# Kernel optimization log

Measured on AMD Instinct MI355X. Metric: run time of the kernel, lower is better.

Reference implementation:

```python
import jax, jax.numpy as jnp
import numpy as np

E = 128          # embed_dim / d_model
DI = 2 * E       # d_inner = expand * d_model = 256
H = 8            # nheads = d_inner / headdim
P = 32           # headdim
N = 64           # d_state
DC = 4           # d_conv
G = 1            # ngroups
XBC = DI + 2 * G * N            # 384
DIN = 2 * DI + 2 * G * N + H    # 648 in_proj width
NL = 4           # number of Mamba2 blocks
PS = 16          # patch size
EPS = 1e-5


def _silu(x):
    return x * jax.nn.sigmoid(x)


def _ln(x, w, b):
    mu = jnp.mean(x, axis=-1, keepdims=True)
    var = jnp.mean(jnp.square(x - mu), axis=-1, keepdims=True)
    return (x - mu) * jax.lax.rsqrt(var + EPS) * w + b


def setup_inputs() -> dict:
    key = jax.random.key(0)
    ks = jax.random.split(key, 20)
    B, IMG = 256, 256
    s = 0.02
    inp = {
        "x": jax.random.normal(ks[0], (B, 3, IMG, IMG), jnp.float32),
        # patch embed conv (E, 3, PS, PS) + bias, then LayerNorm
        "conv_w": jax.random.normal(ks[1], (E, 3, PS, PS), jnp.float32) * s,
        "conv_b": jnp.zeros((E,), jnp.float32),
        "pe_ln_w": jnp.ones((E,), jnp.float32),
        "pe_ln_b": jnp.zeros((E,), jnp.float32),
        # per-block LayerNorms (stacked over NL layers)
        "ln_w": jnp.ones((NL, E), jnp.float32),
        "ln_b": jnp.zeros((NL, E), jnp.float32),
        # Mamba2 params stacked over layers
        "in_w": jax.random.normal(ks[2], (NL, DIN, E), jnp.float32) * s,
        "conv1d_w": jax.random.normal(ks[3], (NL, XBC, DC), jnp.float32) * s,
        "conv1d_b": jnp.zeros((NL, XBC), jnp.float32),
        "dt_bias": jax.random.normal(ks[4], (NL, H), jnp.float32) * 0.5,
        "A_log": jnp.tile(jnp.log(jnp.arange(1, H + 1, dtype=jnp.float32)), (NL, 1)),
        "Dp": jnp.ones((NL, H), jnp.float32),
        "ssm_norm_w": jnp.ones((NL, DI), jnp.float32),
        "out_w": jax.random.normal(ks[5], (NL, E, DI), jnp.float32) * s,
        # final norm + head
        "fn_w": jnp.ones((E,), jnp.float32),
        "fn_b": jnp.zeros((E,), jnp.float32),
        "head_w": jax.random.normal(ks[6], (128, E), jnp.float32) * s,
        "head_b": jnp.zeros((128,), jnp.float32),
    }
    return inp


def _mamba2(x, in_w, cw, cb, dtb, A_log, Dp, nw, ow):
    B, L, _ = x.shape
    zxbcdt = jnp.einsum('ble,de->bld', x, in_w)          # [B,L,648]
    z = zxbcdt[..., :DI]                                  # [B,L,256]
    xbc = zxbcdt[..., DI:DI + XBC]                        # [B,L,384]
    dt = jax.nn.softplus(zxbcdt[..., DI + XBC:] + dtb)    # [B,L,H]
    # causal depthwise conv1d over seq, kernel DC, + silu
    xp = jnp.pad(xbc, ((0, 0), (DC - 1, 0), (0, 0)))
    conv = cb + sum(cw[:, k] * xp[:, k:k + L, :] for k in range(DC))
    xbc = _silu(conv)
    xh = xbc[..., :DI].reshape(B, L, H, P)                # [B,L,H,P]
    Bm = xbc[..., DI:DI + N]                              # [B,L,N] (g=1)
    Cm = xbc[..., DI + N:]                                # [B,L,N]
    A = -jnp.exp(A_log)                                   # [H]
    dA = jnp.exp(dt * A)                                  # [B,L,H]
    # sequential selective scan over L
    def step(h, t):
        dAt, dtt, xt, Bt, Ct = t
        h = dAt[..., None, None] * h + (dtt[..., None] * xt)[..., None] * Bt[:, None, None, :]
        y = jnp.einsum('bhpn,bn->bhp', h, Ct)
        return h, y
    h0 = jnp.zeros((B, H, P, N), x.dtype)
    xs = (jnp.moveaxis(dA, 1, 0), jnp.moveaxis(dt, 1, 0), jnp.moveaxis(xh, 1, 0),
          jnp.moveaxis(Bm, 1, 0), jnp.moveaxis(Cm, 1, 0))
    _, ys = jax.lax.scan(step, h0, xs)                    # [L,B,H,P]
    y = jnp.moveaxis(ys, 0, 1) + Dp[:, None] * xh         # [B,L,H,P]
    y = y.reshape(B, L, DI)
    # gated RMSNorm: rmsnorm(y * silu(z)) * weight
    y = y * _silu(z)
    y = y * jax.lax.rsqrt(jnp.mean(jnp.square(y), axis=-1, keepdims=True) + EPS) * nw
    return jnp.einsum('bld,ed->ble', y, ow)


def reference(x, conv_w, conv_b, pe_ln_w, pe_ln_b, ln_w, ln_b, in_w, conv1d_w,
              conv1d_b, dt_bias, A_log, Dp, ssm_norm_w, out_w, fn_w, fn_b,
              head_w, head_b):
    B = x.shape[0]
    Hh = x.shape[2] // PS
    Ww = x.shape[3] // PS
    # non-overlapping patch conv == blocked einsum
    xp = x.reshape(B, 3, Hh, PS, Ww, PS)
    t = jnp.einsum('bcxpyq,ecpq->bxye', xp, conv_w) + conv_b
    t = t.reshape(B, Hh * Ww, E)                          # [B,L,E]
    t = _ln(t, pe_ln_w, pe_ln_b)
    for i in range(NL):
        t = t + _mamba2(_ln(t, ln_w[i], ln_b[i]), in_w[i], conv1d_w[i],
                        conv1d_b[i], dt_bias[i], A_log[i], Dp[i],
                        ssm_norm_w[i], out_w[i])
    t = _ln(t, fn_w, fn_b)
    t = jnp.mean(t, axis=1)                               # [B,E]
    t = jnp.einsum('be,oe->bo', t, head_w) + head_b       # [B,128]
    nrm = jnp.maximum(jnp.linalg.norm(t, axis=1, keepdims=True), 1e-12)
    return t / nrm
```

## Files before the change

### kernel.cpp

```cpp
#include <hip/hip_runtime.h>
#include <math.h>

#define EE 128
#define DI 256
#define HH 8
#define PP 32
#define NN 64
#define DC 4
#define XBC 384
#define DIN 648
#define NL 4
#define LSEQ 256
#define BB 256
#define TTOK (BB * LSEQ)
#define EPSF 1e-5f

typedef __attribute__((ext_vector_type(8))) short short8;
typedef __attribute__((ext_vector_type(4))) float f32x4;

__device__ inline short f2bf(float f) {
  unsigned u = __builtin_bit_cast(unsigned, f);
  u += 0x7fff + ((u >> 16) & 1);
  return (short)(u >> 16);
}
__device__ inline float bf2f(unsigned short u) {
  unsigned x = ((unsigned)u) << 16;
  return __builtin_bit_cast(float, x);
}
__device__ inline float fast_silu(float a) {
  return a * __builtin_amdgcn_rcpf(1.f + __expf(-a));
}

__global__ __launch_bounds__(256) void cvt_w_kernel(
    const float* __restrict__ in_w, const float* __restrict__ ow,
    unsigned short* __restrict__ in_wb, unsigned short* __restrict__ owb) {
  int i = blockIdx.x * 256 + threadIdx.x;
  in_wb[i] = (unsigned short)f2bf(in_w[i]);
  if (i < NL * EE * DI) owb[i] = (unsigned short)f2bf(ow[i]);
}

__global__ __launch_bounds__(256) void gemm_in_proj(
    const unsigned short* __restrict__ A, const unsigned short* __restrict__ B,
    unsigned short* __restrict__ Czx, float* __restrict__ dtraw,
    int M, int N, int K) {
  __shared__ __align__(16) unsigned short smem[128 * 136];
  short (*As)[40] = (short(*)[40])smem;
  short (*Bs)[40] = (short(*)[40])(smem + 128 * 40);
  const int tid = threadIdx.x;
  const int lane = tid & 63, wid = tid >> 6;
  const int wm = wid >> 1, wn = wid & 1;
  const int m0 = blockIdx.y * 128, n0 = blockIdx.x * 128;
  const int r = tid >> 1, hf = tid & 1;
  const int lr = lane & 15, lk = (lane >> 4) * 8;
  f32x4 acc[4][4] = {};
  for (int k0 = 0; k0 < K; k0 += 32) {
    {
      const unsigned short* ap = A + (size_t)(m0 + r) * K + k0 + hf * 16;
      *(short8*)&As[r][hf * 16] = *(const short8*)(ap);
      *(short8*)&As[r][hf * 16 + 8] = *(const short8*)(ap + 8);
    }
    {
      short8 s0 = {}, s1 = {};
      if (n0 + r < N) {
        const unsigned short* bp = B + (size_t)(n0 + r) * K + k0 + hf * 16;
        s0 = *(const short8*)(bp);
        s1 = *(const short8*)(bp + 8);
      }
      *(short8*)&Bs[r][hf * 16] = s0;
      *(short8*)&Bs[r][hf * 16 + 8] = s1;
    }
    __syncthreads();
    short8 af[4], bfr[4];
#pragma unroll
    for (int mi = 0; mi < 4; ++mi) af[mi] = *(const short8*)&As[wm * 64 + mi * 16 + lr][lk];
#pragma unroll
    for (int ni = 0; ni < 4; ++ni) bfr[ni] = *(const short8*)&Bs[wn * 64 + ni * 16 + lr][lk];
#pragma unroll
    for (int mi = 0; mi < 4; ++mi)
#pragma unroll
      for (int ni = 0; ni < 4; ++ni)
        acc[mi][ni] = __builtin_amdgcn_mfma_f32_16x16x32_bf16(af[mi], bfr[ni], acc[mi][ni], 0, 0, 0);
    __syncthreads();
  }
  {
    unsigned short (*Vt)[136] = (unsigned short(*)[136])smem;
#pragma unroll
    for (int mi = 0; mi < 4; ++mi) {
#pragma unroll
      for (int ni = 0; ni < 4; ++ni) {
        int row0 = wm * 64 + mi * 16 + (lane >> 4) * 4;
        int col = wn * 64 + ni * 16 + lr;
#pragma unroll
        for (int j = 0; j < 4; ++j)
          Vt[row0 + j][col] = (unsigned short)f2bf(acc[mi][ni][j]);
      }
    }
    if (n0 == 640 && wn == 0 && lr < 8) {
#pragma unroll
      for (int mi = 0; mi < 4; ++mi) {
        int row0 = m0 + wm * 64 + mi * 16 + (lane >> 4) * 4;
#pragma unroll
        for (int j = 0; j < 4; ++j)
          dtraw[(size_t)(row0 + j) * 8 + lr] = acc[mi][0][j];
      }
    }
    __syncthreads();
    const int row = tid >> 4, cs = (tid & 15) * 8;
#pragma unroll
    for (int it = 0; it < 8; ++it) {
      int rr2 = it * 16 + row;
      if (n0 + cs < N)
        *(uint4*)(Czx + (size_t)(m0 + rr2) * DIN + n0 + cs) = *(const uint4*)&Vt[rr2][cs];
    }
  }
}

__global__ __launch_bounds__(256) void gemm_out_fused_ln(
    const unsigned short* __restrict__ ysc, const unsigned short* __restrict__ zx,
    const float* __restrict__ nw, const unsigned short* __restrict__ B,
    unsigned short* __restrict__ tres, const float* __restrict__ lnw,
    const float* __restrict__ lnb, unsigned* __restrict__ tnb) {
  __shared__ short As[128][40];
  __shared__ short Bs[128][40];
  __shared__ unsigned short Vt[128][136];
  __shared__ float rs_g[128], mu_s[128], rs_s[128];
  const int tid = threadIdx.x;
  const int lane = tid & 63, wid = tid >> 6;
  const int wm = wid >> 1, wn = wid & 1;
  const int m0 = blockIdx.x * 128;
  const int r = tid >> 1, hf = tid & 1;
  const int lr = lane & 15, lk = (lane >> 4) * 8;
  f32x4 acc[4][4] = {};
  float ssg = 0.f;
  for (int k0 = 0; k0 < 256; k0 += 32) {
    {
      int col = k0 + hf * 16;
      const unsigned short* yp = ysc + (size_t)(m0 + r) * DI + col;
      const unsigned short* zp = zx + (size_t)(m0 + r) * DIN + col;
      short8 y0 = *(const short8*)(yp);
      short8 y1 = *(const short8*)(yp + 8);
      short8 z0 = *(const short8*)(zp);
      short8 z1 = *(const short8*)(zp + 8);
      float4 nw0 = *(const float4*)(nw + col);
      float4 nw1 = *(const float4*)(nw + col + 4);
      float4 nw2 = *(const float4*)(nw + col + 8);
      float4 nw3 = *(const float4*)(nw + col + 12);
      float nwv[16] = {nw0.x, nw0.y, nw0.z, nw0.w, nw1.x, nw1.y, nw1.z, nw1.w,
                       nw2.x, nw2.y, nw2.z, nw2.w, nw3.x, nw3.y, nw3.z, nw3.w};
      short8 a0, a1;
#pragma unroll
      for (int j = 0; j < 8; ++j) {
        float y = bf2f((unsigned short)y0[j]);
        float z = bf2f((unsigned short)z0[j]);
        float g = y * fast_silu(z);
        ssg += g * g;
        a0[j] = f2bf(g * nwv[j]);
        float y2 = bf2f((unsigned short)y1[j]);
        float z2 = bf2f((unsigned short)z1[j]);
        float g2 = y2 * fast_silu(z2);
        ssg += g2 * g2;
        a1[j] = f2bf(g2 * nwv[8 + j]);
      }
      *(short8*)&As[r][hf * 16] = a0;
      *(short8*)&As[r][hf * 16 + 8] = a1;
    }
    {
      const unsigned short* bp = B + (size_t)r * 256 + k0 + hf * 16;
      *(short8*)&Bs[r][hf * 16] = *(const short8*)(bp);
      *(short8*)&Bs[r][hf * 16 + 8] = *(const short8*)(bp + 8);
    }
    __syncthreads();
    short8 af[4], bfr[4];
#pragma unroll
    for (int mi = 0; mi < 4; ++mi) af[mi] = *(const short8*)&As[wm * 64 + mi * 16 + lr][lk];
#pragma unroll
    for (int ni = 0; ni < 4; ++ni) bfr[ni] = *(const short8*)&Bs[wn * 64 + ni * 16 + lr][lk];
#pragma unroll
    for (int mi = 0; mi < 4; ++mi)
#pragma unroll
      for (int ni = 0; ni < 4; ++ni)
        acc[mi][ni] = __builtin_amdgcn_mfma_f32_16x16x32_bf16(af[mi], bfr[ni], acc[mi][ni], 0, 0, 0);
    __syncthreads();
  }
  ssg += __shfl_xor(ssg, 1);
  if (hf == 0) rs_g[r] = rsqrtf(ssg * (1.f / 256.f) + EPSF);
  __syncthreads();
#pragma unroll
  for (int mi = 0; mi < 4; ++mi) {
#pragma unroll
    for (int ni = 0; ni < 4; ++ni) {
      int row0 = wm * 64 + mi * 16 + (lane >> 4) * 4;
      int col = wn * 64 + ni * 16 + lr;
#pragma unroll
      for (int j = 0; j < 4; ++j) {
        int row = row0 + j;
        size_t idx = (size_t)(m0 + row) * 128 + col;
        float v = acc[mi][ni][j] * rs_g[row] + bf2f(tres[idx]);
        unsigned short us = (unsigned short)f2bf(v);
        tres[idx] = us;
        Vt[row][col] = us;
      }
    }
  }
  __syncthreads();
  {
    float s = 0.f, ss = 0.f;
#pragma unroll
    for (int kk = 0; kk < 8; ++kk) {
      short8 vv = *(const short8*)&Vt[r][hf * 64 + kk * 8];
#pragma unroll
      for (int j = 0; j < 8; ++j) {
        float f = bf2f((unsigned short)vv[j]);
        s += f; ss += f * f;
      }
    }
    s += __shfl_xor(s, 1);
    ss += __shfl_xor(ss, 1);
    if (hf == 0) {
      float mu = s * (1.f / 128.f);
      mu_s[r] = mu;
      rs_s[r] = rsqrtf(ss * (1.f / 128.f) - mu * mu + EPSF);
    }
  }
  __syncthreads();
  float w0 = lnw[lane * 2], w1 = lnw[lane * 2 + 1];
  float b0 = lnb[lane * 2], b1 = lnb[lane * 2 + 1];
  for (int it = 0; it < 32; ++it) {
    int row = it * 4 + wid;
    float mu = mu_s[row], rr = rs_s[row];
    float v0 = bf2f(Vt[row][lane * 2]);
    float v1 = bf2f(Vt[row][lane * 2 + 1]);
    unsigned lo = (unsigned short)f2bf((v0 - mu) * rr * w0 + b0);
    unsigned hi = (unsigned short)f2bf((v1 - mu) * rr * w1 + b1);
    tnb[(size_t)(m0 + row) * 64 + lane] = lo | (hi << 16);
  }
}

__global__ __launch_bounds__(256) void gemm_bf16_patch(
    const float* __restrict__ X, const float* __restrict__ B,
    const float* __restrict__ bias, unsigned short* __restrict__ C) {
  __shared__ short As[128][40];
  __shared__ short Bs[128][40];
  const int tid = threadIdx.x;
  const int lane = tid & 63, wid = tid >> 6;
  const int wm = wid >> 1, wn = wid & 1;
  const int m0 = blockIdx.x * 128;
  const int r = tid >> 1, hf = tid & 1;
  const int lr = lane & 15, lk = (lane >> 4) * 8;
  const int m = m0 + r;
  const int bb = m >> 8, px = (m >> 4) & 15, py = m & 15;
  f32x4 acc[4][4] = {};
  for (int k0 = 0; k0 < 768; k0 += 32) {
    int k = k0 + hf * 16;
    int c = k >> 8, dx = (k >> 4) & 15;
    {
      const float* ap = X + (((size_t)(bb * 3 + c) * 256 + px * 16 + dx) * 256 + py * 16);
      float4 v0 = *(const float4*)(ap + 0);
      float4 v1 = *(const float4*)(ap + 4);
      float4 v2 = *(const float4*)(ap + 8);
      float4 v3 = *(const float4*)(ap + 12);
      short8 s0, s1;
      s0[0] = f2bf(v0.x); s0[1] = f2bf(v0.y); s0[2] = f2bf(v0.z); s0[3] = f2bf(v0.w);
      s0[4] = f2bf(v1.x); s0[5] = f2bf(v1.y); s0[6] = f2bf(v1.z); s0[7] = f2bf(v1.w);
      s1[0] = f2bf(v2.x); s1[1] = f2bf(v2.y); s1[2] = f2bf(v2.z); s1[3] = f2bf(v2.w);
      s1[4] = f2bf(v3.x); s1[5] = f2bf(v3.y); s1[6] = f2bf(v3.z); s1[7] = f2bf(v3.w);
      *(short8*)&As[r][hf * 16] = s0;
      *(short8*)&As[r][hf * 16 + 8] = s1;
    }
    {
      const float* bp = B + (size_t)r * 768 + k;
      float4 v0 = *(const float4*)(bp + 0);
      float4 v1 = *(const float4*)(bp + 4);
      float4 v2 = *(const float4*)(bp + 8);
      float4 v3 = *(const float4*)(bp + 12);
      short8 s0, s1;
      s0[0] = f2bf(v0.x); s0[1] = f2bf(v0.y); s0[2] = f2bf(v0.z); s0[3] = f2bf(v0.w);
      s0[4] = f2bf(v1.x); s0[5] = f2bf(v1.y); s0[6] = f2bf(v1.z); s0[7] = f2bf(v1.w);
      s1[0] = f2bf(v2.x); s1[1] = f2bf(v2.y); s1[2] = f2bf(v2.z); s1[3] = f2bf(v2.w);
      s1[4] = f2bf(v3.x); s1[5] = f2bf(v3.y); s1[6] = f2bf(v3.z); s1[7] = f2bf(v3.w);
      *(short8*)&Bs[r][hf * 16] = s0;
      *(short8*)&Bs[r][hf * 16 + 8] = s1;
    }
    __syncthreads();
    short8 af[4], bfr[4];
#pragma unroll
    for (int mi = 0; mi < 4; ++mi) af[mi] = *(const short8*)&As[wm * 64 + mi * 16 + lr][lk];
#pragma unroll
    for (int ni = 0; ni < 4; ++ni) bfr[ni] = *(const short8*)&Bs[wn * 64 + ni * 16 + lr][lk];
#pragma unroll
    for (int mi = 0; mi < 4; ++mi)
#pragma unroll
      for (int ni = 0; ni < 4; ++ni)
        acc[mi][ni] = __builtin_amdgcn_mfma_f32_16x16x32_bf16(af[mi], bfr[ni], acc[mi][ni], 0, 0, 0);
    __syncthreads();
  }
#pragma unroll
  for (int mi = 0; mi < 4; ++mi) {
#pragma unroll
    for (int ni = 0; ni < 4; ++ni) {
      int row0 = m0 + wm * 64 + mi * 16 + (lane >> 4) * 4;
      int col = wn * 64 + ni * 16 + (lane & 15);
#pragma unroll
      for (int j = 0; j < 4; ++j)
        C[(size_t)(row0 + j) * 128 + col] = (unsigned short)f2bf(acc[mi][ni][j] + bias[col]);
    }
  }
}

__global__ __launch_bounds__(256) void ln_pe0_kernel(
    unsigned* t, unsigned* out,
    const float* __restrict__ pe_w, const float* __restrict__ pe_b,
    const float* __restrict__ l0w, const float* __restrict__ l0b) {
  int wid = threadIdx.x >> 6, lane = threadIdx.x & 63;
  size_t token = (size_t)blockIdx.x * 4 + wid;
  unsigned* p = t + token * 64;
  unsigned u = p[lane];
  float vx = bf2f((unsigned short)(u & 0xffff));
  float vy = bf2f((unsigned short)(u >> 16));
  float s = vx + vy;
#pragma unroll
  for (int off = 1; off < 64; off <<= 1) s += __shfl_xor(s, off);
  float mu = s * (1.f / 128.f);
  float dx = vx - mu, dy = vy - mu;
  float vs = dx * dx + dy * dy;
#pragma unroll
  for (int off = 1; off < 64; off <<= 1) vs += __shfl_xor(vs, off);
  float r = rsqrtf(vs * (1.f / 128.f) + EPSF);
  float t0 = dx * r * pe_w[lane * 2 + 0] + pe_b[lane * 2 + 0];
  float t1 = dy * r * pe_w[lane * 2 + 1] + pe_b[lane * 2 + 1];
  unsigned short s0 = (unsigned short)f2bf(t0);
  unsigned short s1 = (unsigned short)f2bf(t1);
  p[lane] = (unsigned)s0 | ((unsigned)s1 << 16);
  float r0 = bf2f(s0), r1 = bf2f(s1);
  float s2 = r0 + r1;
#pragma unroll
  for (int off = 1; off < 64; off <<= 1) s2 += __shfl_xor(s2, off);
  float mu2 = s2 * (1.f / 128.f);
  float d0 = r0 - mu2, d1 = r1 - mu2;
  float vs2 = d0 * d0 + d1 * d1;
#pragma unroll
  for (int off = 1; off < 64; off <<= 1) vs2 += __shfl_xor(vs2, off);
  float r2 = rsqrtf(vs2 * (1.f / 128.f) + EPSF);
  unsigned lo = (unsigned short)f2bf(d0 * r2 * l0w[lane * 2 + 0] + l0b[lane * 2 + 0]);
  unsigned hi = (unsigned short)f2bf(d1 * r2 * l0w[lane * 2 + 1] + l0b[lane * 2 + 1]);
  out[token * 64 + lane] = lo | (hi << 16);
}

__global__ __launch_bounds__(256, 3) void scan_chunk_kernel(
    const unsigned short* __restrict__ zx,
    const float* __restrict__ dtraw,
    const float* __restrict__ dtb,
    const float* __restrict__ A_log,
    const float* __restrict__ cw,
    const float* __restrict__ cbv_g,
    const float* __restrict__ Dp,
    unsigned short* __restrict__ ysc) {
  const int b = blockIdx.x & 255, hp = blockIdx.x >> 8;
  const int h0 = hp * 2;
  const int tid = threadIdx.x;
  const int w = tid >> 6, lane = tid & 63;
  const int lr = lane & 15, lj = lane >> 4;
  __shared__ __align__(16) unsigned short Cb[64][72];
  __shared__ __align__(16) unsigned short Bb[64][72];
  __shared__ __align__(16) unsigned short BbT[64][72];
  __shared__ __align__(16) unsigned short xT0[32][72];
  __shared__ __align__(16) unsigned short xT1[32][72];
  __shared__ __align__(16) unsigned short hbT0[32][72];
  __shared__ __align__(16) unsigned short hbT1[32][72];
  __shared__ float la0[64], la1[64], dtc0[64], dtc1[64], wt0[64], wt1[64];
  for (int i = tid; i < 32 * 72 / 2; i += 256) {
    ((unsigned*)hbT0)[i] = 0;
    ((unsigned*)hbT1)[i] = 0;
  }
  f32x4 acc_h[4] = {};
  const float dph0 = Dp[h0], dph1 = Dp[h0 + 1];
  const int hw = w >> 1;
  const int wrow = (w & 1) * 16;
  __syncthreads();

  for (int c = 0; c < 4; ++c) {
    const int tok0 = b * 256 + c * 64;
    if (w < 2) {
      int hh = h0 + w;
      float raw = dtraw[(size_t)(tok0 + lane) * 8 + hh] + dtb[hh];
      float dt = raw > 20.f ? raw : log1pf(expf(raw));
      float v = -expf(A_log[hh]) * dt;
#pragma unroll
      for (int off = 1; off < 64; off <<= 1) {
        float u = __shfl_up(v, off);
        if (lane >= off) v += u;
      }
      if (w == 0) { la0[lane] = v; dtc0[lane] = dt; }
      else        { la1[lane] = v; dtc1[lane] = dt; }
    }
    for (int it = tid; it < 384; it += 256) {
      int t0, ch, kind, sub;
      if (it < 128) {
        int hx = it >> 6, id = it & 63;
        t0 = (id >> 2) * 4; sub = (id & 3) * 8;
        ch = (h0 + hx) * 32 + sub; kind = hx;
      } else if (it < 256) {
        int id = it - 128;
        t0 = (id >> 3) * 4; sub = (id & 7) * 8;
        ch = 256 + sub; kind = 2;
      } else {
        int id = it - 256;
        t0 = (id >> 3) * 4; sub = (id & 7) * 8;
        ch = 320 + sub; kind = 3;
      }
      const unsigned short* zp = zx + (size_t)(tok0 + t0) * DIN + 256 + ch;
      const int t0loc = c * 64 + t0;
      short8 rr[7];
      if (t0loc >= 3) {
#pragma unroll
        for (int d = 0; d < 7; ++d)
          rr[d] = *(const short8*)(zp + (ptrdiff_t)(d - 3) * DIN);
      } else {
#pragma unroll
        for (int d = 0; d < 7; ++d) {
          short8 z8 = {};
          if (t0loc + d - 3 >= 0) z8 = *(const short8*)(zp + (ptrdiff_t)(d - 3) * DIN);
          rr[d] = z8;
        }
      }
      float4 cwv[8];
      float cbl[8];
#pragma unroll
      for (int j = 0; j < 8; ++j) {
        cwv[j] = *(const float4*)(cw + (ch + j) * 4);
        cbl[j] = cbv_g[ch + j];
      }
      short8 o[4];
#pragma unroll
      for (int tt = 0; tt < 4; ++tt) {
#pragma unroll
        for (int j = 0; j < 8; ++j) {
          float a = cbl[j]
                  + cwv[j].x * bf2f((unsigned short)rr[tt + 0][j])
                  + cwv[j].y * bf2f((unsigned short)rr[tt + 1][j])
                  + cwv[j].z * bf2f((unsigned short)rr[tt + 2][j])
                  + cwv[j].w * bf2f((unsigned short)rr[tt + 3][j]);
          o[tt][j] = f2bf(fast_silu(a));
        }
      }
      if (kind <= 1) {
        unsigned short (*xT)[72] = kind ? xT1 : xT0;
#pragma unroll
        for (int j = 0; j < 8; ++j) {
          ushort4 v;
          v.x = (unsigned short)o[0][j]; v.y = (unsigned short)o[1][j];
          v.z = (unsigned short)o[2][j]; v.w = (unsigned short)o[3][j];
          *(ushort4*)&xT[sub + j][t0] = v;
        }
      } else if (kind == 2) {
        *(short8*)&Bb[t0 + 0][sub] = o[0];
        *(short8*)&Bb[t0 + 1][sub] = o[1];
        *(short8*)&Bb[t0 + 2][sub] = o[2];
        *(short8*)&Bb[t0 + 3][sub] = o[3];
#pragma unroll
        for (int j = 0; j < 8; ++j) {
          ushort4 v;
          v.x = (unsigned short)o[0][j]; v.y = (unsigned short)o[1][j];
          v.z = (unsigned short)o[2][j]; v.w = (unsigned short)o[3][j];
          *(ushort4*)&BbT[sub + j][t0] = v;
        }
      } else {
        *(short8*)&Cb[t0 + 0][sub] = o[0];
        *(short8*)&Cb[t0 + 1][sub] = o[1];
        *(short8*)&Cb[t0 + 2][sub] = o[2];
        *(short8*)&Cb[t0 + 3][sub] = o[3];
      }
    }
    __syncthreads();
    if (w == 3) wt0[lane] = __expf(la0[63] - la0[lane]) * dtc0[lane];
    if (w == 2) wt1[lane] = __expf(la1[63] - la1[lane]) * dtc1[lane];
    short8 afC0 = *(const short8*)&Cb[w * 16 + lr][lj * 8];
    short8 afC1 = *(const short8*)&Cb[w * 16 + lr][32 + lj * 8];
    f32x4 acc_s[4] = {};
#pragma unroll
    for (int ni = 0; ni < 4; ++ni) {
      short8 bf0 = *(const short8*)&Bb[ni * 16 + lr][lj * 8];
      short8 bf1 = *(const short8*)&Bb[ni * 16 + lr][32 + lj * 8];
      acc_s[ni] = __builtin_amdgcn_mfma_f32_16x16x32_bf16(afC0, bf0, acc_s[ni], 0, 0, 0);
      acc_s[ni] = __builtin_amdgcn_mfma_f32_16x16x32_bf16(afC1, bf1, acc_s[ni], 0, 0, 0);
    }
    f32x4 acc_y0[2] = {}, acc_y1[2] = {};
#pragma unroll
    for (int ni = 0; ni < 2; ++ni) {
      short8 hf0 = *(const short8*)&hbT0[ni * 16 + lr][lj * 8];
      short8 hf1 = *(const short8*)&hbT0[ni * 16 + lr][32 + lj * 8];
      acc_y0[ni] = __builtin_amdgcn_mfma_f32_16x16x32_bf16(afC0, hf0, acc_y0[ni], 0, 0, 0);
      acc_y0[ni] = __builtin_amdgcn_mfma_f32_16x16x32_bf16(afC1, hf1, acc_y0[ni], 0, 0, 0);
      short8 gf0 = *(const short8*)&hbT1[ni * 16 + lr][lj * 8];
      short8 gf1 = *(const short8*)&hbT1[ni * 16 + lr][32 + lj * 8];
      acc_y1[ni] = __builtin_amdgcn_mfma_f32_16x16x32_bf16(afC0, gf0, acc_y1[ni], 0, 0, 0);
      acc_y1[ni] = __builtin_amdgcn_mfma_f32_16x16x32_bf16(afC1, gf1, acc_y1[ni], 0, 0, 0);
    }
#pragma unroll
    for (int j = 0; j < 4; ++j) {
      int t = w * 16 + lj * 4 + j;
      float at0 = __expf(la0[t]), at1 = __expf(la1[t]);
      acc_y0[0][j] *= at0; acc_y0[1][j] *= at0;
      acc_y1[0][j] *= at1; acc_y1[1][j] *= at1;
    }
    __syncthreads();
#pragma unroll
    for (int ni = 0; ni < 4; ++ni) {
      int s = ni * 16 + lr;
      float las0 = la0[s], dts0 = dtc0[s];
      float las1 = la1[s], dts1 = dtc1[s];
#pragma unroll
      for (int j = 0; j < 4; ++j) {
        int t = w * 16 + lj * 4 + j;
        float pv0 = 0.f, pv1 = 0.f;
        if (s <= t) {
          pv0 = acc_s[ni][j] * __expf(la0[t] - las0) * dts0;
          pv1 = acc_s[ni][j] * __expf(la1[t] - las1) * dts1;
        }
        Cb[t][s] = (unsigned short)f2bf(pv0);
        Bb[t][s] = (unsigned short)f2bf(pv1);
      }
    }
    __syncthreads();
    {
      short8 aP0a = *(const short8*)&Cb[w * 16 + lr][lj * 8];
      short8 aP0b = *(const short8*)&Cb[w * 16 + lr][32 + lj * 8];
      short8 aP1a = *(const short8*)&Bb[w * 16 + lr][lj * 8];
      short8 aP1b = *(const short8*)&Bb[w * 16 + lr][32 + lj * 8];
#pragma unroll
      for (int ni = 0; ni < 2; ++ni) {
        short8 x0a = *(const short8*)&xT0[ni * 16 + lr][lj * 8];
        short8 x0b = *(const short8*)&xT0[ni * 16 + lr][32 + lj * 8];
        acc_y0[ni] = __builtin_amdgcn_mfma_f32_16x16x32_bf16(aP0a, x0a, acc_y0[ni], 0, 0, 0);
        acc_y0[ni] = __builtin_amdgcn_mfma_f32_16x16x32_bf16(aP0b, x0b, acc_y0[ni], 0, 0, 0);
        short8 x1a = *(const short8*)&xT1[ni * 16 + lr][lj * 8];
        short8 x1b = *(const short8*)&xT1[ni * 16 + lr][32 + lj * 8];
        acc_y1[ni] = __builtin_amdgcn_mfma_f32_16x16x32_bf16(aP1a, x1a, acc_y1[ni], 0, 0, 0);
        acc_y1[ni] = __builtin_amdgcn_mfma_f32_16x16x32_bf16(aP1b, x1b, acc_y1[ni], 0, 0, 0);
      }
    }
    {
      const float* laP = hw ? la1 : la0;
      const float* wtP = hw ? wt1 : wt0;
      unsigned short (*xTP)[72] = hw ? xT1 : xT0;
      float aend = __expf(laP[63]);
#pragma unroll
      for (int ni = 0; ni < 4; ++ni)
#pragma unroll
        for (int j = 0; j < 4; ++j) acc_h[ni][j] *= aend;
#pragma unroll
      for (int kk = 0; kk < 2; ++kk) {
        short8 xv = *(const short8*)&xTP[wrow + lr][kk * 32 + lj * 8];
        short8 axf;
#pragma unroll
        for (int j = 0; j < 8; ++j)
          axf[j] = f2bf(bf2f((unsigned short)xv[j]) * wtP[kk * 32 + lj * 8 + j]);
#pragma unroll
        for (int ni = 0; ni < 4; ++ni) {
          short8 bw = *(const short8*)&BbT[ni * 16 + lr][kk * 32 + lj * 8];
          acc_h[ni] = __builtin_amdgcn_mfma_f32_16x16x32_bf16(axf, bw, acc_h[ni], 0, 0, 0);
        }
      }
    }
#pragma unroll
    for (int ni = 0; ni < 2; ++ni) {
#pragma unroll
      for (int j = 0; j < 4; ++j) {
        int t = w * 16 + lj * 4 + j;
        int p = ni * 16 + lr;
        size_t base = (size_t)(tok0 + t) * DI;
        float yv0 = acc_y0[ni][j] + dph0 * bf2f(xT0[p][t]);
        ysc[base + h0 * 32 + p] = (unsigned short)f2bf(yv0);
        float yv1 = acc_y1[ni][j] + dph1 * bf2f(xT1[p][t]);
        ysc[base + (h0 + 1) * 32 + p] = (unsigned short)f2bf(yv1);
      }
    }
    {
      unsigned short (*hbTP)[72] = hw ? hbT1 : hbT0;
#pragma unroll
      for (int ni = 0; ni < 4; ++ni)
#pragma unroll
        for (int j = 0; j < 4; ++j)
          hbTP[wrow + lj * 4 + j][ni * 16 + lr] = (unsigned short)f2bf(acc_h[ni][j]);
    }
    __syncthreads();
  }
}

__global__ __launch_bounds__(128) void head_kernel(
    const unsigned short* __restrict__ tn, const float* __restrict__ hw,
    const float* __restrict__ hb, float* __restrict__ out) {
  __shared__ float tm[128];
  __shared__ float red[2];
  int b = blockIdx.x, o = threadIdx.x;
  {
    const unsigned short* p = tn + (size_t)b * 256 * 128 + o;
    float acc = 0.f;
    for (int l = 0; l < 256; ++l) acc += bf2f(p[l * 128]);
    tm[o] = acc * (1.f / 256.f);
  }
  __syncthreads();
  float acc = hb[o];
  for (int e = 0; e < 128; ++e) acc += tm[e] * hw[o * 128 + e];
  float ss = acc * acc;
#pragma unroll
  for (int off = 1; off < 64; off <<= 1) ss += __shfl_xor(ss, off);
  if ((o & 63) == 0) red[o >> 6] = ss;
  __syncthreads();
  float nrm = fmaxf(sqrtf(red[0] + red[1]), 1e-12f);
  out[b * 128 + o] = acc / nrm;
}

extern "C" void kernel_launch(void* const* d_in, const int* in_sizes, int n_in,
                              void* d_out, int out_size, void* d_ws, size_t ws_size,
                              hipStream_t stream) {
  const float* x      = (const float*)d_in[0];
  const float* conv_w = (const float*)d_in[1];
  const float* conv_b = (const float*)d_in[2];
  const float* pe_w   = (const float*)d_in[3];
  const float* pe_b   = (const float*)d_in[4];
  const float* ln_w   = (const float*)d_in[5];
  const float* ln_b   = (const float*)d_in[6];
  const float* in_w   = (const float*)d_in[7];
  const float* c1w    = (const float*)d_in[8];
  const float* c1b    = (const float*)d_in[9];
  const float* dtb    = (const float*)d_in[10];
  const float* A_log  = (const float*)d_in[11];
  const float* Dp     = (const float*)d_in[12];
  const float* nw     = (const float*)d_in[13];
  const float* ow     = (const float*)d_in[14];
  const float* fn_w   = (const float*)d_in[15];
  const float* fn_b   = (const float*)d_in[16];
  const float* hw     = (const float*)d_in[17];
  const float* hb     = (const float*)d_in[18];
  float* out = (float*)d_out;

  const size_t T = TTOK;
  char* w8 = (char*)d_ws;
  unsigned short* t_buf = (unsigned short*)w8;   w8 += T * 128 * 2;
  unsigned*       tnb   = (unsigned*)w8;         w8 += T * 128 * 2;
  unsigned short* zx    = (unsigned short*)w8;   w8 += T * (size_t)DIN * 2;
  float*          dtraw = (float*)w8;            w8 += T * 8 * 4;
  unsigned short* ysc   = (unsigned short*)w8;   w8 += T * (size_t)DI * 2;
  unsigned short* in_wb = (unsigned short*)w8;   w8 += (size_t)NL * DIN * EE * 2;
  unsigned short* owb   = (unsigned short*)w8;   w8 += (size_t)NL * EE * DI * 2;
  if ((size_t)(w8 - (char*)d_ws) > ws_size) return;

  cvt_w_kernel<<<1296, 256, 0, stream>>>(in_w, ow, in_wb, owb);

  gemm_bf16_patch<<<dim3(512, 1), 256, 0, stream>>>(x, conv_w, conv_b, t_buf);
  ln_pe0_kernel<<<16384, 256, 0, stream>>>((unsigned*)t_buf, tnb, pe_w, pe_b, ln_w, ln_b);

  for (int i = 0; i < NL; ++i) {
    gemm_in_proj<<<dim3(6, 512), 256, 0, stream>>>(
        (const unsigned short*)tnb, in_wb + (size_t)i * DIN * EE, zx, dtraw, TTOK, DIN, EE);
    scan_chunk_kernel<<<1024, 256, 0, stream>>>(
        zx, dtraw, dtb + i * HH, A_log + i * HH,
        c1w + (size_t)i * XBC * DC, c1b + (size_t)i * XBC, Dp + i * HH, ysc);
    const float* nlw = (i < NL - 1) ? (ln_w + (i + 1) * 128) : fn_w;
    const float* nlb = (i < NL - 1) ? (ln_b + (i + 1) * 128) : fn_b;
    gemm_out_fused_ln<<<512, 256, 0, stream>>>(
        ysc, zx, nw + i * DI, owb + (size_t)i * EE * DI, t_buf, nlw, nlb, tnb);
  }

  head_kernel<<<256, 128, 0, stream>>>((const unsigned short*)tnb, hw, hb, out);
}
```

Before: 642.4 us.

## Process four heads per scan block to reuse B/C conv and CB product

The chunked scan kernel now handles four heads per block instead of two, halving the grid to 512 blocks. The B and C conv1d+silu work and the C·B^T score matrix are computed once per four heads rather than per two, which cuts redundant loads and MFMA work. Each wave now owns one head's state update, with twice the accumulators, and the intra-chunk pass is split into two rounds with extra barriers. Shared memory and register use grow, so the occupancy hint drops from 3 to 2 blocks per CU, and the smaller grid may underfill the GPU.

Measured after the change: 588.6 us. 1.09x faster.

```diff
diff --git a/kernel.cpp b/kernel.cpp
--- a/kernel.cpp
+++ b/kernel.cpp
@@ -346,7 +346,7 @@
   out[token * 64 + lane] = lo | (hi << 16);
 }
 
-__global__ __launch_bounds__(256, 3) void scan_chunk_kernel(
+__global__ __launch_bounds__(256, 2) void scan_chunk_kernel(
     const unsigned short* __restrict__ zx,
     const float* __restrict__ dtraw,
     const float* __restrict__ dtb,
@@ -355,32 +355,25 @@
     const float* __restrict__ cbv_g,
     const float* __restrict__ Dp,
     unsigned short* __restrict__ ysc) {
-  const int b = blockIdx.x & 255, hp = blockIdx.x >> 8;
-  const int h0 = hp * 2;
+  const int b = blockIdx.x & 255, hq = blockIdx.x >> 8;
+  const int h0 = hq * 4;
   const int tid = threadIdx.x;
   const int w = tid >> 6, lane = tid & 63;
   const int lr = lane & 15, lj = lane >> 4;
   __shared__ __align__(16) unsigned short Cb[64][72];
   __shared__ __align__(16) unsigned short Bb[64][72];
   __shared__ __align__(16) unsigned short BbT[64][72];
-  __shared__ __align__(16) unsigned short xT0[32][72];
-  __shared__ __align__(16) unsigned short xT1[32][72];
-  __shared__ __align__(16) unsigned short hbT0[32][72];
-  __shared__ __align__(16) unsigned short hbT1[32][72];
-  __shared__ float la0[64], la1[64], dtc0[64], dtc1[64], wt0[64], wt1[64];
-  for (int i = tid; i < 32 * 72 / 2; i += 256) {
-    ((unsigned*)hbT0)[i] = 0;
-    ((unsigned*)hbT1)[i] = 0;
-  }
-  f32x4 acc_h[4] = {};
-  const float dph0 = Dp[h0], dph1 = Dp[h0 + 1];
-  const int hw = w >> 1;
-  const int wrow = (w & 1) * 16;
+  __shared__ __align__(16) unsigned short xT[4][32][72];
+  __shared__ __align__(16) unsigned short hbT[4][32][72];
+  __shared__ float la[4][64], dtc[4][64], wt[4][64];
+  for (int i = tid; i < 4608; i += 256) ((unsigned*)hbT)[i] = 0;
+  f32x4 acc_h[8] = {};
+  const float dp0 = Dp[h0], dp1 = Dp[h0 + 1], dp2 = Dp[h0 + 2], dp3 = Dp[h0 + 3];
   __syncthreads();
 
   for (int c = 0; c < 4; ++c) {
     const int tok0 = b * 256 + c * 64;
-    if (w < 2) {
+    {
       int hh = h0 + w;
       float raw = dtraw[(size_t)(tok0 + lane) * 8 + hh] + dtb[hh];
       float dt = raw > 20.f ? raw : log1pf(expf(raw));
@@ -390,23 +383,23 @@
         float u = __shfl_up(v, off);
         if (lane >= off) v += u;
       }
-      if (w == 0) { la0[lane] = v; dtc0[lane] = dt; }
-      else        { la1[lane] = v; dtc1[lane] = dt; }
-    }
-    for (int it = tid; it < 384; it += 256) {
+      la[w][lane] = v;
+      dtc[w][lane] = dt;
+    }
+    for (int it = tid; it < 512; it += 256) {
       int t0, ch, kind, sub;
-      if (it < 128) {
+      if (it < 256) {
         int hx = it >> 6, id = it & 63;
         t0 = (id >> 2) * 4; sub = (id & 3) * 8;
         ch = (h0 + hx) * 32 + sub; kind = hx;
-      } else if (it < 256) {
-        int id = it - 128;
-        t0 = (id >> 3) * 4; sub = (id & 7) * 8;
-        ch = 256 + sub; kind = 2;
-      } else {
+      } else if (it < 384) {
         int id = it - 256;
         t0 = (id >> 3) * 4; sub = (id & 7) * 8;
-        ch = 320 + sub; kind = 3;
+        ch = 256 + sub; kind = 4;
+      } else {
+        int id = it - 384;
+        t0 = (id >> 3) * 4; sub = (id & 7) * 8;
+        ch = 320 + sub; kind = 5;
       }
       const unsigned short* zp = zx + (size_t)(tok0 + t0) * DIN + 256 + ch;
       const int t0loc = c * 64 + t0;
@@ -443,16 +436,15 @@
           o[tt][j] = f2bf(fast_silu(a));
         }
       }
-      if (kind <= 1) {
-        unsigned short (*xT)[72] = kind ? xT1 : xT0;
+      if (kind < 4) {
 #pragma unroll
         for (int j = 0; j < 8; ++j) {
           ushort4 v;
           v.x = (unsigned short)o[0][j]; v.y = (unsigned short)o[1][j];
           v.z = (unsigned short)o[2][j]; v.w = (unsigned short)o[3][j];
-          *(ushort4*)&xT[sub + j][t0] = v;
-        }
-      } else if (kind == 2) {
+          *(ushort4*)&xT[kind][sub + j][t0] = v;
+        }
+      } else if (kind == 4) {
         *(short8*)&Bb[t0 + 0][sub] = o[0];
         *(short8*)&Bb[t0 + 1][sub] = o[1];
         *(short8*)&Bb[t0 + 2][sub] = o[2];
@@ -472,8 +464,7 @@
       }
     }
     __syncthreads();
-    if (w == 3) wt0[lane] = __expf(la0[63] - la0[lane]) * dtc0[lane];
-    if (w == 2) wt1[lane] = __expf(la1[63] - la1[lane]) * dtc1[lane];
+    wt[w][lane] = __expf(la[w][63] - la[w][lane]) * dtc[w][lane];
     short8 afC0 = *(const short8*)&Cb[w * 16 + lr][lj * 8];
     short8 afC1 = *(const short8*)&Cb[w * 16 + lr][32 + lj * 8];
     f32x4 acc_s[4] = {};
@@ -484,38 +475,63 @@
       acc_s[ni] = __builtin_amdgcn_mfma_f32_16x16x32_bf16(afC0, bf0, acc_s[ni], 0, 0, 0);
       acc_s[ni] = __builtin_amdgcn_mfma_f32_16x16x32_bf16(afC1, bf1, acc_s[ni], 0, 0, 0);
     }
-    f32x4 acc_y0[2] = {}, acc_y1[2] = {};
-#pragma unroll
-    for (int ni = 0; ni < 2; ++ni) {
-      short8 hf0 = *(const short8*)&hbT0[ni * 16 + lr][lj * 8];
-      short8 hf1 = *(const short8*)&hbT0[ni * 16 + lr][32 + lj * 8];
-      acc_y0[ni] = __builtin_amdgcn_mfma_f32_16x16x32_bf16(afC0, hf0, acc_y0[ni], 0, 0, 0);
-      acc_y0[ni] = __builtin_amdgcn_mfma_f32_16x16x32_bf16(afC1, hf1, acc_y0[ni], 0, 0, 0);
-      short8 gf0 = *(const short8*)&hbT1[ni * 16 + lr][lj * 8];
-      short8 gf1 = *(const short8*)&hbT1[ni * 16 + lr][32 + lj * 8];
-      acc_y1[ni] = __builtin_amdgcn_mfma_f32_16x16x32_bf16(afC0, gf0, acc_y1[ni], 0, 0, 0);
-      acc_y1[ni] = __builtin_amdgcn_mfma_f32_16x16x32_bf16(afC1, gf1, acc_y1[ni], 0, 0, 0);
+    f32x4 acc_y[4][2] = {};
+#pragma unroll
+    for (int hh = 0; hh < 4; ++hh) {
+#pragma unroll
+      for (int ni = 0; ni < 2; ++ni) {
+        short8 hf0 = *(const short8*)&hbT[hh][ni * 16 + lr][lj * 8];
+        short8 hf1 = *(const short8*)&hbT[hh][ni * 16 + lr][32 + lj * 8];
+        acc_y[hh][ni] = __builtin_amdgcn_mfma_f32_16x16x32_bf16(afC0, hf0, acc_y[hh][ni], 0, 0, 0);
+        acc_y[hh][ni] = __builtin_amdgcn_mfma_f32_16x16x32_bf16(afC1, hf1, acc_y[hh][ni], 0, 0, 0);
+      }
     }
 #pragma unroll
     for (int j = 0; j < 4; ++j) {
       int t = w * 16 + lj * 4 + j;
-      float at0 = __expf(la0[t]), at1 = __expf(la1[t]);
-      acc_y0[0][j] *= at0; acc_y0[1][j] *= at0;
-      acc_y1[0][j] *= at1; acc_y1[1][j] *= at1;
+#pragma unroll
+      for (int hh = 0; hh < 4; ++hh) {
+        float at = __expf(la[hh][t]);
+        acc_y[hh][0][j] *= at;
+        acc_y[hh][1][j] *= at;
+      }
+    }
+    {
+      float aend = __expf(la[w][63]);
+#pragma unroll
+      for (int f = 0; f < 8; ++f)
+#pragma unroll
+        for (int j = 0; j < 4; ++j) acc_h[f][j] *= aend;
+#pragma unroll
+      for (int kk = 0; kk < 2; ++kk) {
+#pragma unroll
+        for (int rh = 0; rh < 2; ++rh) {
+          short8 xv = *(const short8*)&xT[w][rh * 16 + lr][kk * 32 + lj * 8];
+          short8 axf;
+#pragma unroll
+          for (int j = 0; j < 8; ++j)
+            axf[j] = f2bf(bf2f((unsigned short)xv[j]) * wt[w][kk * 32 + lj * 8 + j]);
+#pragma unroll
+          for (int ni = 0; ni < 4; ++ni) {
+            short8 bw = *(const short8*)&BbT[ni * 16 + lr][kk * 32 + lj * 8];
+            acc_h[rh * 4 + ni] = __builtin_amdgcn_mfma_f32_16x16x32_bf16(axf, bw, acc_h[rh * 4 + ni], 0, 0, 0);
+          }
+        }
+      }
     }
     __syncthreads();
 #pragma unroll
     for (int ni = 0; ni < 4; ++ni) {
       int s = ni * 16 + lr;
-      float las0 = la0[s], dts0 = dtc0[s];
-      float las1 = la1[s], dts1 = dtc1[s];
+      float las0 = la[0][s], dts0 = dtc[0][s];
+      float las1 = la[1][s], dts1 = dtc[1][s];
 #pragma unroll
       for (int j = 0; j < 4; ++j) {
         int t = w * 16 + lj * 4 + j;
         float pv0 = 0.f, pv1 = 0.f;
         if (s <= t) {
-          pv0 = acc_s[ni][j] * __expf(la0[t] - las0) * dts0;
-          pv1 = acc_s[ni][j] * __expf(la1[t] - las1) * dts1;
+          pv0 = acc_s[ni][j] * __expf(la[0][t] - las0) * dts0;
+          pv1 = acc_s[ni][j] * __expf(la[1][t] - las1) * dts1;
         }
         Cb[t][s] = (unsigned short)f2bf(pv0);
         Bb[t][s] = (unsigned short)f2bf(pv1);
@@ -529,60 +545,85 @@
       short8 aP1b = *(const short8*)&Bb[w * 16 + lr][32 + lj * 8];
 #pragma unroll
       for (int ni = 0; ni < 2; ++ni) {
-        short8 x0a = *(const short8*)&xT0[ni * 16 + lr][lj * 8];
-        short8 x0b = *(const short8*)&xT0[ni * 16 + lr][32 + lj * 8];
-        acc_y0[ni] = __builtin_amdgcn_mfma_f32_16x16x32_bf16(aP0a, x0a, acc_y0[ni], 0, 0, 0);
-        acc_y0[ni] = __builtin_amdgcn_mfma_f32_16x16x32_bf16(aP0b, x0b, acc_y0[ni], 0, 0, 0);
-        short8 x1a = *(const short8*)&xT1[ni * 16 + lr][lj * 8];
-        short8 x1b = *(const short8*)&xT1[ni * 16 + lr][32 + lj * 8];
-        acc_y1[ni] = __builtin_amdgcn_mfma_f32_16x16x32_bf16(aP1a, x1a, acc_y1[ni], 0, 0, 0);
-        acc_y1[ni] = __builtin_amdgcn_mfma_f32_16x16x32_bf16(aP1b, x1b, acc_y1[ni], 0, 0, 0);
-      }
-    }
-    {
-      const float* laP = hw ? la1 : la0;
-      const float* wtP = hw ? wt1 : wt0;
-      unsigned short (*xTP)[72] = hw ? xT1 : xT0;
-      float aend = __expf(laP[63]);
-#pragma unroll
-      for (int ni = 0; ni < 4; ++ni)
-#pragma unroll
-        for (int j = 0; j < 4; ++j) acc_h[ni][j] *= aend;
-#pragma unroll
-      for (int kk = 0; kk < 2; ++kk) {
-        short8 xv = *(const short8*)&xTP[wrow + lr][kk * 32 + lj * 8];
-        short8 axf;
-#pragma unroll
-        for (int j = 0; j < 8; ++j)
-          axf[j] = f2bf(bf2f((unsigned short)xv[j]) * wtP[kk * 32 + lj * 8 + j]);
-#pragma unroll
-        for (int ni = 0; ni < 4; ++ni) {
-          short8 bw = *(const short8*)&BbT[ni * 16 + lr][kk * 32 + lj * 8];
-          acc_h[ni] = __builtin_amdgcn_mfma_f32_16x16x32_bf16(axf, bw, acc_h[ni], 0, 0, 0);
-        }
-      }
-    }
-#pragma unroll
-    for (int ni = 0; ni < 2; ++ni) {
+        short8 x0a = *(const short8*)&xT[0][ni * 16 + lr][lj * 8];
+        short8 x0b = *(const short8*)&xT[0][ni * 16 + lr][32 + lj * 8];
+        acc_y[0][ni] = __builtin_amdgcn_mfma_f32_16x16x32_bf16(aP0a, x0a, acc_y[0][ni], 0, 0, 0);
+        acc_y[0][ni] = __builtin_amdgcn_mfma_f32_16x16x32_bf16(aP0b, x0b, acc_y[0][ni], 0, 0, 0);
+        short8 x1a = *(const short8*)&xT[1][ni * 16 + lr][lj * 8];
+        short8 x1b = *(const short8*)&xT[1][ni * 16 + lr][32 + lj * 8];
+        acc_y[1][ni] = __builtin_amdgcn_mfma_f32_16x16x32_bf16(aP1a, x1a, acc_y[1][ni], 0, 0, 0);
+        acc_y[1][ni] = __builtin_amdgcn_mfma_f32_16x16x32_bf16(aP1b, x1b, acc_y[1][ni], 0, 0, 0);
+      }
+#pragma unroll
+      for (int ni = 0; ni < 2; ++ni) {
+#pragma unroll
+        for (int j = 0; j < 4; ++j) {
+          int t = w * 16 + lj * 4 + j;
+          int p = ni * 16 + lr;
+          size_t base = (size_t)(tok0 + t) * DI;
+          float yv0 = acc_y[0][ni][j] + dp0 * bf2f(xT[0][p][t]);
+          ysc[base + (h0 + 0) * 32 + p] = (unsigned short)f2bf(yv0);
+          float yv1 = acc_y[1][ni][j] + dp1 * bf2f(xT[1][p][t]);
+          ysc[base + (h0 + 1) * 32 + p] = (unsigned short)f2bf(yv1);
+        }
+      }
+    }
+    __syncthreads();
+#pragma unroll
+    for (int ni = 0; ni < 4; ++ni) {
+      int s = ni * 16 + lr;
+      float las2 = la[2][s], dts2 = dtc[2][s];
+      float las3 = la[3][s], dts3 = dtc[3][s];
 #pragma unroll
       for (int j = 0; j < 4; ++j) {
         int t = w * 16 + lj * 4 + j;
-        int p = ni * 16 + lr;
-        size_t base = (size_t)(tok0 + t) * DI;
-        float yv0 = acc_y0[ni][j] + dph0 * bf2f(xT0[p][t]);
-        ysc[base + h0 * 32 + p] = (unsigned short)f2bf(yv0);
-        float yv1 = acc_y1[ni][j] + dph1 * bf2f(xT1[p][t]);
-        ysc[base + (h0 + 1) * 32 + p] = (unsigned short)f2bf(yv1);
-      }
-    }
-    {
-      unsigned short (*hbTP)[72] = hw ? hbT1 : hbT0;
+        float pv2 = 0.f, pv3 = 0.f;
+        if (s <= t) {
+          pv2 = acc_s[ni][j] * __expf(la[2][t] - las2) * dts2;
+          pv3 = acc_s[ni][j] * __expf(la[3][t] - las3) * dts3;
+        }
+        Cb[t][s] = (unsigned short)f2bf(pv2);
+        Bb[t][s] = (unsigned short)f2bf(pv3);
+      }
+    }
+    __syncthreads();
+    {
+      short8 aP2a = *(const short8*)&Cb[w * 16 + lr][lj * 8];
+      short8 aP2b = *(const short8*)&Cb[w * 16 + lr][32 + lj * 8];
+      short8 aP3a = *(const short8*)&Bb[w * 16 + lr][lj * 8];
+      short8 aP3b = *(const short8*)&Bb[w * 16 + lr][32 + lj * 8];
+#pragma unroll
+      for (int ni = 0; ni < 2; ++ni) {
+        short8 x2a = *(const short8*)&xT[2][ni * 16 + lr][lj * 8];
+        short8 x2b = *(const short8*)&xT[2][ni * 16 + lr][32 + lj * 8];
+        acc_y[2][ni] = __builtin_amdgcn_mfma_f32_16x16x32_bf16(aP2a, x2a, acc_y[2][ni], 0, 0, 0);
+        acc_y[2][ni] = __builtin_amdgcn_mfma_f32_16x16x32_bf16(aP2b, x2b, acc_y[2][ni], 0, 0, 0);
+        short8 x3a = *(const short8*)&xT[3][ni * 16 + lr][lj * 8];
+        short8 x3b = *(const short8*)&xT[3][ni * 16 + lr][32 + lj * 8];
+        acc_y[3][ni] = __builtin_amdgcn_mfma_f32_16x16x32_bf16(aP3a, x3a, acc_y[3][ni], 0, 0, 0);
+        acc_y[3][ni] = __builtin_amdgcn_mfma_f32_16x16x32_bf16(aP3b, x3b, acc_y[3][ni], 0, 0, 0);
+      }
+#pragma unroll
+      for (int ni = 0; ni < 2; ++ni) {
+#pragma unroll
+        for (int j = 0; j < 4; ++j) {
+          int t = w * 16 + lj * 4 + j;
+          int p = ni * 16 + lr;
+          size_t base = (size_t)(tok0 + t) * DI;
+          float yv2 = acc_y[2][ni][j] + dp2 * bf2f(xT[2][p][t]);
+          ysc[base + (h0 + 2) * 32 + p] = (unsigned short)f2bf(yv2);
+          float yv3 = acc_y[3][ni][j] + dp3 * bf2f(xT[3][p][t]);
+          ysc[base + (h0 + 3) * 32 + p] = (unsigned short)f2bf(yv3);
+        }
+      }
+    }
+#pragma unroll
+    for (int rh = 0; rh < 2; ++rh)
 #pragma unroll
       for (int ni = 0; ni < 4; ++ni)
 #pragma unroll
         for (int j = 0; j < 4; ++j)
-          hbTP[wrow + lj * 4 + j][ni * 16 + lr] = (unsigned short)f2bf(acc_h[ni][j]);
-    }
+          hbT[w][rh * 16 + lj * 4 + j][ni * 16 + lr] = (unsigned short)f2bf(acc_h[rh * 4 + ni][j]);
     __syncthreads();
   }
 }
@@ -654,7 +695,7 @@
   for (int i = 0; i < NL; ++i) {
     gemm_in_proj<<<dim3(6, 512), 256, 0, stream>>>(
         (const unsigned short*)tnb, in_wb + (size_t)i * DIN * EE, zx, dtraw, TTOK, DIN, EE);
-    scan_chunk_kernel<<<1024, 256, 0, stream>>>(
+    scan_chunk_kernel<<<512, 256, 0, stream>>>(
         zx, dtraw, dtb + i * HH, A_log + i * HH,
         c1w + (size_t)i * XBC * DC, c1b + (size_t)i * XBC, Dp + i * HH, ysc);
     const float* nlw = (i < NL - 1) ? (ln_w + (i + 1) * 128) : fn_w;
```
